# Kernel optimization log

Measured on AMD Instinct MI355X. Metric: run time of the kernel, lower is better.

## Reference

```python
import jax, jax.numpy as jnp
import numpy as np

B, T, H, IN = 64, 2048, 256, 6
TH_X = 0.0  # DeltaJANET hard-codes thx=0 into the rnn layer
TH_H = 0.0


def setup_inputs() -> dict:
    key = jax.random.key(0)
    ks = jax.random.split(key, 4)
    return {
        "x": jax.random.normal(ks[0], (B, T, 2), dtype=jnp.float32),
        "h_0": jnp.zeros((1, B, H), dtype=jnp.float32),
        "weight_ih": jax.random.normal(ks[1], (2 * H, IN), dtype=jnp.float32) * 0.2,
        "weight_hh": jax.random.normal(ks[2], (2 * H, H), dtype=jnp.float32) * 0.05,
        "bias_ih": jnp.zeros((2 * H,), dtype=jnp.float32),
        "bias_hh": jnp.zeros((2 * H,), dtype=jnp.float32),
        "fc_w": jax.random.normal(ks[3], (2, H), dtype=jnp.float32) * 0.05,
        "fc_b": jnp.zeros((2,), dtype=jnp.float32),
    }


def _features(x):
    i_x = x[..., 0:1]
    q_x = x[..., 1:2]
    amp = jnp.sqrt(i_x * i_x + q_x * q_x)
    amp3 = amp ** 3
    cos = i_x / amp
    sin = q_x / amp
    return jnp.concatenate((i_x, q_x, amp, amp3, sin, cos), axis=-1)  # [B,T,6]


def reference(x, h_0, weight_ih, weight_hh, bias_ih, bias_hh, fc_w, fc_b):
    feats = _features(x)                       # [B,T,6]
    xs = jnp.swapaxes(feats, 0, 1)             # [T,B,6] time-major
    b = x.shape[0]
    h0 = jnp.zeros((b, H), feats.dtype)        # h_0 arg is ignored (set to None in torch forward)
    dm0 = jnp.broadcast_to(bias_ih + bias_hh, (b, 2 * H)).astype(feats.dtype)
    x_p0 = jnp.zeros((b, IN), feats.dtype)

    def step(carry, x_t):
        x_p, h, h_p, dm = carry
        dx_raw = x_t - x_p
        dh_raw = h - h_p
        dx_abs = jnp.abs(dx_raw)
        dh_abs = jnp.abs(dh_raw)
        dx = jnp.where(dx_abs < TH_X, 0.0, dx_raw)
        dh = jnp.where(dh_abs < TH_H, 0.0, dh_raw)
        x_p_n = jnp.where(dx_abs >= TH_X, x_t, x_p)
        h_p_n = jnp.where(dh_abs >= TH_H, h, h_p)
        mac_x = dx @ weight_ih.T + dm           # [B,2H]
        mac_h = dh @ weight_hh.T                # [B,2H]
        dm_f = mac_x[:, :H] + mac_h[:, :H]
        dm_g = mac_x[:, H:] + mac_h[:, H:]
        dm_n = jnp.concatenate((dm_f, dm_g), axis=1)
        gate_f = jax.nn.sigmoid(dm_f)
        gate_g = jax.nn.sigmoid(dm_g)
        h_n = (1.0 - gate_f) * gate_g + gate_f * h
        return (x_p_n, h_n, h_p_n, dm_n), h_n

    _, hs = jax.lax.scan(step, (x_p0, h0, h0, dm0), xs)  # hs: [T,B,H]
    out = jnp.swapaxes(hs, 0, 1)               # [B,T,H]
    return out @ fc_w.T + fc_b                 # [B,T,2]
```

## Files before the change

### kernel.cpp

```cpp
#include <hip/hip_runtime.h>
#include <math.h>

typedef _Float16 half2v __attribute__((ext_vector_type(2)));

#define TT 2048
#define CH 20

#if __has_builtin(__builtin_amdgcn_fdot2)
#define FDOT2(a,b,c) __builtin_amdgcn_fdot2((a),(b),(c),false)
#else
#define FDOT2(a,b,c) ((c) + (float)(a).x*(float)(b).x + (float)(a).y*(float)(b).y)
#endif

__global__ __launch_bounds__(1024, 4)
void janet_rnn(const float* __restrict__ x,
               const float* __restrict__ w_ih,
               const float* __restrict__ w_hh,
               const float* __restrict__ b_ih,
               const float* __restrict__ b_hh,
               const float* __restrict__ fc_w,
               const float* __restrict__ fc_b,
               float* __restrict__ out)
{
    __shared__ unsigned int hbuf[2][8 * CH];
    __shared__ float dm[512];
    __shared__ float fcw[512];

    const int tid = threadIdx.x;
    const int b   = blockIdx.x;
    const int cc  = tid & 7;
    const int rg  = tid >> 3;
    const int r0  = rg * 4;
    const int c0  = cc * 32;

    if (tid < 8 * CH) { hbuf[0][tid] = 0u; hbuf[1][tid] = 0u; }
    if (tid < 512) fcw[tid] = fc_w[tid];

    half2v wp[4][16];
    #pragma unroll
    for (int i = 0; i < 4; ++i) {
        const float* wr = w_hh + (r0 + i) * 256 + c0;
        #pragma unroll
        for (int j = 0; j < 8; ++j) {
            const float4 v = *reinterpret_cast<const float4*>(wr + j * 4);
            half2v p0; p0.x = (_Float16)v.x; p0.y = (_Float16)v.y;
            half2v p1; p1.x = (_Float16)v.z; p1.y = (_Float16)v.w;
            wp[i][j * 2 + 0] = p0;
            wp[i][j * 2 + 1] = p1;
        }
    }

    float wf[6], wg[6], bsf = 0.f, bsg = 0.f;
    if (tid < 256) {
        #pragma unroll
        for (int c = 0; c < 6; ++c) {
            wf[c] = w_ih[tid * 6 + c];
            wg[c] = w_ih[(256 + tid) * 6 + c];
        }
        bsf = b_ih[tid]       + b_hh[tid];
        bsg = b_ih[256 + tid] + b_hh[256 + tid];
    }
    const int pl = tid - 256;
    const float fcb0 = fc_b[0], fcb1 = fc_b[1];

    float hreg = 0.0f;

    const float* xb   = x   + (size_t)b * TT * 2;
    float*       outb = out + (size_t)b * TT * 2;

    __syncthreads();

    #pragma unroll 1
    for (int t = 0; t < TT; ++t) {
        float xi = 0.f, xq = 0.f;
        if (tid < 256) {
            const float2 xv = *reinterpret_cast<const float2*>(xb + 2 * t);
            xi = xv.x; xq = xv.y;
        }

        const unsigned int* hb = &hbuf[(t + 1) & 1][cc * CH];
        float a0 = 0.f, a1 = 0.f, a2 = 0.f, a3 = 0.f;
        #pragma unroll
        for (int q = 0; q < 4; ++q) {
            const uint4 r = *reinterpret_cast<const uint4*>(hb + 4 * q);
            const half2v h0 = __builtin_bit_cast(half2v, r.x);
            const half2v h1 = __builtin_bit_cast(half2v, r.y);
            const half2v h2 = __builtin_bit_cast(half2v, r.z);
            const half2v h3 = __builtin_bit_cast(half2v, r.w);
            a0 = FDOT2(wp[0][q*4+0], h0, a0); a0 = FDOT2(wp[0][q*4+1], h1, a0);
            a0 = FDOT2(wp[0][q*4+2], h2, a0); a0 = FDOT2(wp[0][q*4+3], h3, a0);
            a1 = FDOT2(wp[1][q*4+0], h0, a1); a1 = FDOT2(wp[1][q*4+1], h1, a1);
            a1 = FDOT2(wp[1][q*4+2], h2, a1); a1 = FDOT2(wp[1][q*4+3], h3, a1);
            a2 = FDOT2(wp[2][q*4+0], h0, a2); a2 = FDOT2(wp[2][q*4+1], h1, a2);
            a2 = FDOT2(wp[2][q*4+2], h2, a2); a2 = FDOT2(wp[2][q*4+3], h3, a2);
            a3 = FDOT2(wp[3][q*4+0], h0, a3); a3 = FDOT2(wp[3][q*4+1], h1, a3);
            a3 = FDOT2(wp[3][q*4+2], h2, a3); a3 = FDOT2(wp[3][q*4+3], h3, a3);
        }
        a0 += __shfl_xor(a0, 1); a0 += __shfl_xor(a0, 2); a0 += __shfl_xor(a0, 4);
        a1 += __shfl_xor(a1, 1); a1 += __shfl_xor(a1, 2); a1 += __shfl_xor(a1, 4);
        a2 += __shfl_xor(a2, 1); a2 += __shfl_xor(a2, 2); a2 += __shfl_xor(a2, 4);
        a3 += __shfl_xor(a3, 1); a3 += __shfl_xor(a3, 2); a3 += __shfl_xor(a3, 4);
        if (cc == 0)
            *reinterpret_cast<float4*>(&dm[r0]) = make_float4(a0, a1, a2, a3);
        __syncthreads();

        if (tid < 256) {
            const float amp  = sqrtf(xi * xi + xq * xq);
            const float amp3 = amp * amp * amp;
            const float snv  = xq / amp;
            const float csv  = xi / amp;
            float dmf = dm[tid]       + bsf;
            float dmg = dm[256 + tid] + bsg;
            dmf += wf[0]*xi + wf[1]*xq + wf[2]*amp + wf[3]*amp3 + wf[4]*snv + wf[5]*csv;
            dmg += wg[0]*xi + wg[1]*xq + wg[2]*amp + wg[3]*amp3 + wg[4]*snv + wg[5]*csv;
            const float gf = 1.0f / (1.0f + __expf(-dmf));
            const float gg = 1.0f / (1.0f + __expf(-dmg));
            hreg = (1.0f - gf) * gg + gf * hreg;
            const float hhi = __shfl_down(hreg, 1);
            if ((tid & 1) == 0) {
                half2v hp2; hp2.x = (_Float16)hreg; hp2.y = (_Float16)hhi;
                const int d = tid >> 1;
                hbuf[t & 1][(d >> 4) * CH + (d & 15)] =
                    __builtin_bit_cast(unsigned int, hp2);
            }
        } else if (pl < 64 && t > 0) {
            const unsigned int* hp = hbuf[(t + 1) & 1];
            const int d0 = 2 * pl, d1 = 2 * pl + 1;
            const half2v ha = __builtin_bit_cast(half2v, hp[(d0 >> 4) * CH + (d0 & 15)]);
            const half2v hc = __builtin_bit_cast(half2v, hp[(d1 >> 4) * CH + (d1 & 15)]);
            const float h0v = (float)ha.x, h1v = (float)ha.y;
            const float h2v = (float)hc.x, h3v = (float)hc.y;
            const float4 w0 = *reinterpret_cast<const float4*>(&fcw[4 * pl]);
            const float4 w1 = *reinterpret_cast<const float4*>(&fcw[256 + 4 * pl]);
            float po0 = w0.x*h0v + w0.y*h1v + w0.z*h2v + w0.w*h3v;
            float po1 = w1.x*h0v + w1.y*h1v + w1.z*h2v + w1.w*h3v;
            #pragma unroll
            for (int s = 1; s < 64; s <<= 1) {
                po0 += __shfl_xor(po0, s);
                po1 += __shfl_xor(po1, s);
            }
            if (pl == 0)
                *reinterpret_cast<float2*>(outb + (t - 1) * 2) =
                    make_float2(po0 + fcb0, po1 + fcb1);
        }
        __syncthreads();
    }

    if (pl >= 0 && pl < 64) {
        const unsigned int* hp = hbuf[(TT - 1) & 1];
        const int d0 = 2 * pl, d1 = 2 * pl + 1;
        const half2v ha = __builtin_bit_cast(half2v, hp[(d0 >> 4) * CH + (d0 & 15)]);
        const half2v hc = __builtin_bit_cast(half2v, hp[(d1 >> 4) * CH + (d1 & 15)]);
        const float h0v = (float)ha.x, h1v = (float)ha.y;
        const float h2v = (float)hc.x, h3v = (float)hc.y;
        const float4 w0 = *reinterpret_cast<const float4*>(&fcw[4 * pl]);
        const float4 w1 = *reinterpret_cast<const float4*>(&fcw[256 + 4 * pl]);
        float po0 = w0.x*h0v + w0.y*h1v + w0.z*h2v + w0.w*h3v;
        float po1 = w1.x*h0v + w1.y*h1v + w1.z*h2v + w1.w*h3v;
        #pragma unroll
        for (int s = 1; s < 64; s <<= 1) {
            po0 += __shfl_xor(po0, s);
            po1 += __shfl_xor(po1, s);
        }
        if (pl == 0)
            *reinterpret_cast<float2*>(outb + (TT - 1) * 2) =
                make_float2(po0 + fcb0, po1 + fcb1);
    }
}

extern "C" void kernel_launch(void* const* d_in, const int* in_sizes, int n_in,
                              void* d_out, int out_size, void* d_ws, size_t ws_size,
                              hipStream_t stream) {
    (void)in_sizes; (void)n_in; (void)out_size; (void)d_ws; (void)ws_size;
    const float* x    = (const float*)d_in[0];
    const float* w_ih = (const float*)d_in[2];
    const float* w_hh = (const float*)d_in[3];
    const float* b_ih = (const float*)d_in[4];
    const float* b_hh = (const float*)d_in[5];
    const float* fc_w = (const float*)d_in[6];
    const float* fc_b = (const float*)d_in[7];
    float* outp = (float*)d_out;

    hipLaunchKernelGGL(janet_rnn, dim3(64), dim3(1024), 0, stream,
                       x, w_ih, w_hh, b_ih, b_hh, fc_w, fc_b, outp);
}
```

Measured before the change: 2.904 ms.

## Rewrite recurrence as batched MFMA over 16 sequences per block

Replaces the one-sequence-per-block fdot2 recurrence with a kernel where each block processes 16 batch elements and computes the hidden-state matvec as 16x16x32 fp16 MFMAs. The input projection and bias are folded into extra K columns (features plus a constant-one column), and the FC output is computed by the MFMA pipeline one step behind. The grid shrinks from 64 blocks to 4, which removes per-step shuffle reductions and one barrier per step, but leaves only 4 CUs busy and makes each step's latency bound to the serial MFMA chain. The input features and bias now also pass through fp16, which changes numerics.

```diff
diff --git a/kernel.cpp b/kernel.cpp
--- a/kernel.cpp
+++ b/kernel.cpp
@@ -1,170 +1,192 @@
 #include <hip/hip_runtime.h>
 #include <math.h>
 
+typedef _Float16 f16x8 __attribute__((ext_vector_type(8)));
+typedef float    f32x4 __attribute__((ext_vector_type(4)));
 typedef _Float16 half2v __attribute__((ext_vector_type(2)));
 
-#define TT 2048
-#define CH 20
-
-#if __has_builtin(__builtin_amdgcn_fdot2)
-#define FDOT2(a,b,c) __builtin_amdgcn_fdot2((a),(b),(c),false)
-#else
-#define FDOT2(a,b,c) ((c) + (float)(a).x*(float)(b).x + (float)(a).y*(float)(b).y)
-#endif
-
-__global__ __launch_bounds__(1024, 4)
-void janet_rnn(const float* __restrict__ x,
-               const float* __restrict__ w_ih,
-               const float* __restrict__ w_hh,
-               const float* __restrict__ b_ih,
-               const float* __restrict__ b_hh,
-               const float* __restrict__ fc_w,
-               const float* __restrict__ fc_b,
-               float* __restrict__ out)
+#define TT   2048
+#define ROWB 640
+
+
+__global__ __launch_bounds__(512, 2)
+void janet_mfma(const float* __restrict__ x,
+                const float* __restrict__ w_ih,
+                const float* __restrict__ w_hh,
+                const float* __restrict__ b_ih,
+                const float* __restrict__ b_hh,
+                const float* __restrict__ fc_w,
+                const float* __restrict__ fc_b,
+                float* __restrict__ out)
 {
-    __shared__ unsigned int hbuf[2][8 * CH];
-    __shared__ float dm[512];
-    __shared__ float fcw[512];
-
-    const int tid = threadIdx.x;
-    const int b   = blockIdx.x;
-    const int cc  = tid & 7;
-    const int rg  = tid >> 3;
-    const int r0  = rg * 4;
-    const int c0  = cc * 32;
-
-    if (tid < 8 * CH) { hbuf[0][tid] = 0u; hbuf[1][tid] = 0u; }
-    if (tid < 512) fcw[tid] = fc_w[tid];
-
-    half2v wp[4][16];
+    __shared__ __align__(16) unsigned char Hb[2][16][ROWB];
+    __shared__ float pout[2][8][16][2];
+
+    const int tid  = threadIdx.x;
+    const int wid  = tid >> 6;
+    const int lane = tid & 63;
+    const int c    = lane & 15;
+    const int hi   = lane >> 4;
+    const int swz  = (c & 7) << 4;
+    const int b0   = blockIdx.x * 16;
+
+    for (int i = tid; i < (2 * 16 * ROWB) / 4; i += 512) ((unsigned int*)Hb)[i] = 0u;
+    ((float*)pout)[tid] = 0.f;
+    __syncthreads();
+    if (tid < 32) {
+        const int p = tid >> 4, cc = tid & 15;
+        const int sz = (cc & 7) << 4;
+        *(unsigned short*)((unsigned char*)&Hb[p][cc][0] + (524 ^ sz)) = 0x3C00;
+    }
+
+    auto wval = [&](int r, int k) -> float {
+        if (r < 512) {
+            if (k < 256) return w_hh[r * 256 + k];
+            if (k < 262) return w_ih[r * 6 + (k - 256)];
+            if (k == 262) return b_ih[r] + b_hh[r];
+            return 0.f;
+        } else if (r < 514) {
+            const int o = r - 512;
+            if (k < 256) return fc_w[o * 256 + k];
+            if (k == 262) return fc_b[o];
+            return 0.f;
+        }
+        return 0.f;
+    };
+
+    const int mt[4] = {2 * wid, 2 * wid + 1, 2 * wid + 16, 2 * wid + 17};
+    f16x8 A[4][9];
     #pragma unroll
     for (int i = 0; i < 4; ++i) {
-        const float* wr = w_hh + (r0 + i) * 256 + c0;
+        const int r = 16 * mt[i] + c;
         #pragma unroll
-        for (int j = 0; j < 8; ++j) {
-            const float4 v = *reinterpret_cast<const float4*>(wr + j * 4);
-            half2v p0; p0.x = (_Float16)v.x; p0.y = (_Float16)v.y;
-            half2v p1; p1.x = (_Float16)v.z; p1.y = (_Float16)v.w;
-            wp[i][j * 2 + 0] = p0;
-            wp[i][j * 2 + 1] = p1;
-        }
-    }
-
-    float wf[6], wg[6], bsf = 0.f, bsg = 0.f;
-    if (tid < 256) {
+        for (int s = 0; s < 8; ++s) {
+            const float4 v0 = *reinterpret_cast<const float4*>(&w_hh[r * 256 + s * 32 + hi * 8]);
+            const float4 v1 = *reinterpret_cast<const float4*>(&w_hh[r * 256 + s * 32 + hi * 8 + 4]);
+            f16x8 a;
+            a[0]=(_Float16)v0.x; a[1]=(_Float16)v0.y; a[2]=(_Float16)v0.z; a[3]=(_Float16)v0.w;
+            a[4]=(_Float16)v1.x; a[5]=(_Float16)v1.y; a[6]=(_Float16)v1.z; a[7]=(_Float16)v1.w;
+            A[i][s] = a;
+        }
+        {
+            f16x8 a;
+            #pragma unroll
+            for (int j = 0; j < 8; ++j) a[j] = (_Float16)wval(r, 256 + hi * 8 + j);
+            A[i][8] = a;
+        }
+    }
+    f16x8 Aout, Aout8;
+    #pragma unroll
+    for (int j = 0; j < 8; ++j) Aout[j] = (_Float16)wval(512 + c, wid * 32 + hi * 8 + j);
+    #pragma unroll
+    for (int j = 0; j < 8; ++j) Aout8[j] = (_Float16)wval(512 + c, 256 + hi * 8 + j);
+
+    float hold[2][4] = {{0.f,0.f,0.f,0.f},{0.f,0.f,0.f,0.f}};
+
+    const float* xb = x + ((size_t)(b0 + c)) * TT * 2;
+
+    __syncthreads();
+    if (wid == 0 && lane < 16) {
+        const float2 xv = *reinterpret_cast<const float2*>(xb + 0);
+        const float amp = sqrtf(xv.x * xv.x + xv.y * xv.y);
+        unsigned char* dst = (unsigned char*)&Hb[1][lane][0];
+        half2v f01; f01.x = (_Float16)xv.x;        f01.y = (_Float16)xv.y;
+        half2v f23; f23.x = (_Float16)amp;         f23.y = (_Float16)(amp*amp*amp);
+        half2v f45; f45.x = (_Float16)(xv.y/amp);  f45.y = (_Float16)(xv.x/amp);
+        *(unsigned int*)(dst + (512 ^ swz)) = __builtin_bit_cast(unsigned int, f01);
+        *(unsigned int*)(dst + (516 ^ swz)) = __builtin_bit_cast(unsigned int, f23);
+        *(unsigned int*)(dst + (520 ^ swz)) = __builtin_bit_cast(unsigned int, f45);
+    }
+    __syncthreads();
+
+    #pragma unroll 1
+    for (int t = 0; t <= TT; ++t) {
+        const int p_read  = (t + 1) & 1;
+        const int p_write = t & 1;
+
+        float2 xv;
+        if (wid == 0 && lane < 16 && t + 1 < TT)
+            xv = *reinterpret_cast<const float2*>(xb + 2 * (t + 1));
+
+        const unsigned char* hrow = (const unsigned char*)&Hb[p_read][c][0];
+        f32x4 C0 = {0,0,0,0}, C1 = {0,0,0,0}, C2 = {0,0,0,0}, C3 = {0,0,0,0};
+        f32x4 Cout = {0,0,0,0};
+        const int doMain = (t < TT);
         #pragma unroll
-        for (int c = 0; c < 6; ++c) {
-            wf[c] = w_ih[tid * 6 + c];
-            wg[c] = w_ih[(256 + tid) * 6 + c];
-        }
-        bsf = b_ih[tid]       + b_hh[tid];
-        bsg = b_ih[256 + tid] + b_hh[256 + tid];
-    }
-    const int pl = tid - 256;
-    const float fcb0 = fc_b[0], fcb1 = fc_b[1];
-
-    float hreg = 0.0f;
-
-    const float* xb   = x   + (size_t)b * TT * 2;
-    float*       outb = out + (size_t)b * TT * 2;
-
-    __syncthreads();
-
-    #pragma unroll 1
-    for (int t = 0; t < TT; ++t) {
-        float xi = 0.f, xq = 0.f;
-        if (tid < 256) {
-            const float2 xv = *reinterpret_cast<const float2*>(xb + 2 * t);
-            xi = xv.x; xq = xv.y;
-        }
-
-        const unsigned int* hb = &hbuf[(t + 1) & 1][cc * CH];
-        float a0 = 0.f, a1 = 0.f, a2 = 0.f, a3 = 0.f;
+        for (int s = 0; s < 9; ++s) {
+            const f16x8 Bs = *(const f16x8*)(hrow + ((s * 64 + hi * 16) ^ swz));
+            if (doMain) {
+                C0 = __builtin_amdgcn_mfma_f32_16x16x32_f16(A[0][s], Bs, C0, 0, 0, 0);
+                C1 = __builtin_amdgcn_mfma_f32_16x16x32_f16(A[1][s], Bs, C1, 0, 0, 0);
+                C2 = __builtin_amdgcn_mfma_f32_16x16x32_f16(A[2][s], Bs, C2, 0, 0, 0);
+                C3 = __builtin_amdgcn_mfma_f32_16x16x32_f16(A[3][s], Bs, C3, 0, 0, 0);
+            }
+            if (s == wid)
+                Cout = __builtin_amdgcn_mfma_f32_16x16x32_f16(Aout, Bs, Cout, 0, 0, 0);
+            if (wid == 0 && s == 8)
+                Cout = __builtin_amdgcn_mfma_f32_16x16x32_f16(Aout8, Bs, Cout, 0, 0, 0);
+        }
+
+        if (doMain) {
+            unsigned char* dstrow = (unsigned char*)&Hb[p_write][c][0];
+            #pragma unroll
+            for (int pp = 0; pp < 2; ++pp) {
+                const f32x4 f = (pp == 0) ? C0 : C1;
+                const f32x4 g = (pp == 0) ? C2 : C3;
+                float hn[4];
+                #pragma unroll
+                for (int r = 0; r < 4; ++r) {
+                    const float gf = 1.0f / (1.0f + __expf(-f[r]));
+                    const float gg = 1.0f / (1.0f + __expf(-g[r]));
+                    hn[r] = gg + gf * (hold[pp][r] - gg);
+                    hold[pp][r] = hn[r];
+                }
+                half2v lo; lo.x = (_Float16)hn[0]; lo.y = (_Float16)hn[1];
+                half2v hp; hp.x = (_Float16)hn[2]; hp.y = (_Float16)hn[3];
+                uint2 v; v.x = __builtin_bit_cast(unsigned int, lo);
+                         v.y = __builtin_bit_cast(unsigned int, hp);
+                const int r0 = 16 * mt[pp] + hi * 4;
+                *(uint2*)(dstrow + ((2 * r0) ^ swz)) = v;
+            }
+        }
+
+        if (wid == 0 && lane < 16 && t + 1 < TT) {
+            const float amp = sqrtf(xv.x * xv.x + xv.y * xv.y);
+            unsigned char* dst = (unsigned char*)&Hb[p_write][lane][0];
+            half2v f01; f01.x = (_Float16)xv.x;        f01.y = (_Float16)xv.y;
+            half2v f23; f23.x = (_Float16)amp;         f23.y = (_Float16)(amp*amp*amp);
+            half2v f45; f45.x = (_Float16)(xv.y/amp);  f45.y = (_Float16)(xv.x/amp);
+            *(unsigned int*)(dst + (512 ^ swz)) = __builtin_bit_cast(unsigned int, f01);
+            *(unsigned int*)(dst + (516 ^ swz)) = __builtin_bit_cast(unsigned int, f23);
+            *(unsigned int*)(dst + (520 ^ swz)) = __builtin_bit_cast(unsigned int, f45);
+        }
+
+        if (hi == 0) {
+            float2 po; po.x = Cout[0]; po.y = Cout[1];
+            *(float2*)&pout[p_read][wid][c][0] = po;
+        }
+        if (wid == 1 && lane < 16 && t >= 2) {
+            float s0 = 0.f, s1 = 0.f;
+            #pragma unroll
+            for (int w = 0; w < 8; ++w) {
+                s0 += pout[p_write][w][lane][0];
+                s1 += pout[p_write][w][lane][1];
+            }
+            *reinterpret_cast<float2*>(out + ((size_t)(b0 + lane) * TT + (t - 2)) * 2) =
+                make_float2(s0, s1);
+        }
+        __syncthreads();
+    }
+
+    if (wid == 1 && lane < 16) {
+        float s0 = 0.f, s1 = 0.f;
         #pragma unroll
-        for (int q = 0; q < 4; ++q) {
-            const uint4 r = *reinterpret_cast<const uint4*>(hb + 4 * q);
-            const half2v h0 = __builtin_bit_cast(half2v, r.x);
-            const half2v h1 = __builtin_bit_cast(half2v, r.y);
-            const half2v h2 = __builtin_bit_cast(half2v, r.z);
-            const half2v h3 = __builtin_bit_cast(half2v, r.w);
-            a0 = FDOT2(wp[0][q*4+0], h0, a0); a0 = FDOT2(wp[0][q*4+1], h1, a0);
-            a0 = FDOT2(wp[0][q*4+2], h2, a0); a0 = FDOT2(wp[0][q*4+3], h3, a0);
-            a1 = FDOT2(wp[1][q*4+0], h0, a1); a1 = FDOT2(wp[1][q*4+1], h1, a1);
-            a1 = FDOT2(wp[1][q*4+2], h2, a1); a1 = FDOT2(wp[1][q*4+3], h3, a1);
-            a2 = FDOT2(wp[2][q*4+0], h0, a2); a2 = FDOT2(wp[2][q*4+1], h1, a2);
-            a2 = FDOT2(wp[2][q*4+2], h2, a2); a2 = FDOT2(wp[2][q*4+3], h3, a2);
-            a3 = FDOT2(wp[3][q*4+0], h0, a3); a3 = FDOT2(wp[3][q*4+1], h1, a3);
-            a3 = FDOT2(wp[3][q*4+2], h2, a3); a3 = FDOT2(wp[3][q*4+3], h3, a3);
-        }
-        a0 += __shfl_xor(a0, 1); a0 += __shfl_xor(a0, 2); a0 += __shfl_xor(a0, 4);
-        a1 += __shfl_xor(a1, 1); a1 += __shfl_xor(a1, 2); a1 += __shfl_xor(a1, 4);
-        a2 += __shfl_xor(a2, 1); a2 += __shfl_xor(a2, 2); a2 += __shfl_xor(a2, 4);
-        a3 += __shfl_xor(a3, 1); a3 += __shfl_xor(a3, 2); a3 += __shfl_xor(a3, 4);
-        if (cc == 0)
-            *reinterpret_cast<float4*>(&dm[r0]) = make_float4(a0, a1, a2, a3);
-        __syncthreads();
-
-        if (tid < 256) {
-            const float amp  = sqrtf(xi * xi + xq * xq);
-            const float amp3 = amp * amp * amp;
-            const float snv  = xq / amp;
-            const float csv  = xi / amp;
-            float dmf = dm[tid]       + bsf;
-            float dmg = dm[256 + tid] + bsg;
-            dmf += wf[0]*xi + wf[1]*xq + wf[2]*amp + wf[3]*amp3 + wf[4]*snv + wf[5]*csv;
-            dmg += wg[0]*xi + wg[1]*xq + wg[2]*amp + wg[3]*amp3 + wg[4]*snv + wg[5]*csv;
-            const float gf = 1.0f / (1.0f + __expf(-dmf));
-            const float gg = 1.0f / (1.0f + __expf(-dmg));
-            hreg = (1.0f - gf) * gg + gf * hreg;
-            const float hhi = __shfl_down(hreg, 1);
-            if ((tid & 1) == 0) {
-                half2v hp2; hp2.x = (_Float16)hreg; hp2.y = (_Float16)hhi;
-                const int d = tid >> 1;
-                hbuf[t & 1][(d >> 4) * CH + (d & 15)] =
-                    __builtin_bit_cast(unsigned int, hp2);
-            }
-        } else if (pl < 64 && t > 0) {
-            const unsigned int* hp = hbuf[(t + 1) & 1];
-            const int d0 = 2 * pl, d1 = 2 * pl + 1;
-            const half2v ha = __builtin_bit_cast(half2v, hp[(d0 >> 4) * CH + (d0 & 15)]);
-            const half2v hc = __builtin_bit_cast(half2v, hp[(d1 >> 4) * CH + (d1 & 15)]);
-            const float h0v = (float)ha.x, h1v = (float)ha.y;
-            const float h2v = (float)hc.x, h3v = (float)hc.y;
-            const float4 w0 = *reinterpret_cast<const float4*>(&fcw[4 * pl]);
-            const float4 w1 = *reinterpret_cast<const float4*>(&fcw[256 + 4 * pl]);
-            float po0 = w0.x*h0v + w0.y*h1v + w0.z*h2v + w0.w*h3v;
-            float po1 = w1.x*h0v + w1.y*h1v + w1.z*h2v + w1.w*h3v;
-            #pragma unroll
-            for (int s = 1; s < 64; s <<= 1) {
-                po0 += __shfl_xor(po0, s);
-                po1 += __shfl_xor(po1, s);
-            }
-            if (pl == 0)
-                *reinterpret_cast<float2*>(outb + (t - 1) * 2) =
-                    make_float2(po0 + fcb0, po1 + fcb1);
-        }
-        __syncthreads();
-    }
-
-    if (pl >= 0 && pl < 64) {
-        const unsigned int* hp = hbuf[(TT - 1) & 1];
-        const int d0 = 2 * pl, d1 = 2 * pl + 1;
-        const half2v ha = __builtin_bit_cast(half2v, hp[(d0 >> 4) * CH + (d0 & 15)]);
-        const half2v hc = __builtin_bit_cast(half2v, hp[(d1 >> 4) * CH + (d1 & 15)]);
-        const float h0v = (float)ha.x, h1v = (float)ha.y;
-        const float h2v = (float)hc.x, h3v = (float)hc.y;
-        const float4 w0 = *reinterpret_cast<const float4*>(&fcw[4 * pl]);
-        const float4 w1 = *reinterpret_cast<const float4*>(&fcw[256 + 4 * pl]);
-        float po0 = w0.x*h0v + w0.y*h1v + w0.z*h2v + w0.w*h3v;
-        float po1 = w1.x*h0v + w1.y*h1v + w1.z*h2v + w1.w*h3v;
-        #pragma unroll
-        for (int s = 1; s < 64; s <<= 1) {
-            po0 += __shfl_xor(po0, s);
-            po1 += __shfl_xor(po1, s);
-        }
-        if (pl == 0)
-            *reinterpret_cast<float2*>(outb + (TT - 1) * 2) =
-                make_float2(po0 + fcb0, po1 + fcb1);
+        for (int w = 0; w < 8; ++w) {
+            s0 += pout[(TT + 1) & 1][w][lane][0];
+            s1 += pout[(TT + 1) & 1][w][lane][1];
+        }
+        *reinterpret_cast<float2*>(out + ((size_t)(b0 + lane) * TT + (TT - 1)) * 2) =
+            make_float2(s0, s1);
     }
 }
 
@@ -181,6 +203,6 @@
     const float* fc_b = (const float*)d_in[7];
     float* outp = (float*)d_out;
 
-    hipLaunchKernelGGL(janet_rnn, dim3(64), dim3(1024), 0, stream,
+    hipLaunchKernelGGL(janet_mfma, dim3(4), dim3(512), 0, stream,
                        x, w_ih, w_hh, b_ih, b_hh, fc_w, fc_b, outp);
 }
```

Result: slower. 3.517 ms (+21.1%).
